# Performance work log

Hardware: AMD Instinct MI355X
Metric: run time of the kernel (lower is better)

## Reference

```python
import jax, jax.numpy as jnp
import numpy as np

# Model dims
L, B, S, D, H, V = 8, 4, 1024, 1024, 16, 256
FF = 4 * D
LN_EPS = 1e-5


def _ln(x, g, b):
    mu = jnp.mean(x, axis=-1, keepdims=True)
    var = jnp.mean(jnp.square(x - mu), axis=-1, keepdims=True)
    return (x - mu) * jax.lax.rsqrt(var + LN_EPS) * g + b


def setup_inputs() -> dict:
    key = jax.random.key(0)
    ks = jax.random.split(key, 12)
    p = lambda k, shape: (jax.random.normal(k, shape, jnp.float32) * 0.02)
    return {
        "input_tokens": jax.random.randint(ks[0], (B, S), 0, V),
        "tok_emb": p(ks[1], (V, D)),
        "pos_emb": p(ks[2], (S, D)),
        "Wq": p(ks[3], (L, D, D)),
        "Wk": p(ks[4], (L, D, D)),
        "Wv": p(ks[5], (L, D, D)),
        "Wo": p(ks[6], (L, D, D)),
        "bo": jnp.zeros((L, D), jnp.float32),
        "ln1_g": jnp.ones((L, D), jnp.float32),
        "ln1_b": jnp.zeros((L, D), jnp.float32),
        "ln2_g": jnp.ones((L, D), jnp.float32),
        "ln2_b": jnp.zeros((L, D), jnp.float32),
        "W1": p(ks[7], (L, D, FF)),
        "b1": jnp.zeros((L, FF), jnp.float32),
        "W2": p(ks[8], (L, FF, D)),
        "b2": jnp.zeros((L, D), jnp.float32),
        "lnf_g": jnp.ones((D,), jnp.float32),
        "lnf_b": jnp.zeros((D,), jnp.float32),
        "Wout": p(ks[9], (D, V)),
        "bout": jnp.zeros((V,), jnp.float32),
        "nhead": 16,
    }


def reference(input_tokens, tok_emb, pos_emb, Wq, Wk, Wv, Wo, bo,
              ln1_g, ln1_b, ln2_g, ln2_b, W1, b1, W2, b2,
              lnf_g, lnf_b, Wout, bout, nhead):
    b, s = input_tokens.shape
    d = tok_emb.shape[-1]
    hd = d // nhead
    scale = jnp.asarray(hd, jnp.float32) ** -0.5  # head_size ** -0.5
    mask = jnp.tril(jnp.ones((s, s), bool))  # causal

    x = tok_emb[input_tokens] + pos_emb[:s][None]  # [b,s,d]

    def block(x, p):
        wq, wk, wv, wo, bo_, g1, be1, g2, be2, w1, bf1, w2, bf2 = p
        h = _ln(x, g1, be1)
        q = (h @ wq).reshape(b, s, nhead, hd)
        k = (h @ wk).reshape(b, s, nhead, hd)
        v = (h @ wv).reshape(b, s, nhead, hd)
        scores = jnp.einsum('bqhd,bkhd->bhqk', q, k) * scale
        scores = jnp.where(mask, scores, -jnp.inf)
        attn = jax.nn.softmax(scores, axis=-1)  # dropout is identity (p=0 / eval)
        o = jnp.einsum('bhqk,bkhd->bqhd', attn, v).reshape(b, s, d)
        x = x + o @ wo + bo_
        h2 = _ln(x, g2, be2)
        x = x + jax.nn.relu(h2 @ w1 + bf1) @ w2 + bf2
        return x, None

    x, _ = jax.lax.scan(block, x, (Wq, Wk, Wv, Wo, bo, ln1_g, ln1_b,
                                   ln2_g, ln2_b, W1, b1, W2, b2))
    logits = _ln(x, lnf_g, lnf_b) @ Wout + bout  # [b,s,V]
    return logits
```

## Files before the change

### kernel.cpp

```cpp
#include <hip/hip_runtime.h>

#define DEV __device__ __forceinline__

typedef __bf16 bf16x8 __attribute__((ext_vector_type(8)));
typedef float  f32x4  __attribute__((ext_vector_type(4)));

typedef const __attribute__((address_space(1))) unsigned int* gas_ptr;
typedef       __attribute__((address_space(3))) unsigned int* las_ptr;

DEV unsigned short f2bf(float f) {
  union { __bf16 h; unsigned short u; } c; c.h = (__bf16)f; return c.u;
}

DEV float bf2f(unsigned short u) {
  union { unsigned int i; float f; } c; c.i = (unsigned int)u << 16; return c.f;
}

DEV void gll16(const void* g, void* l) {
  __builtin_amdgcn_global_load_lds((gas_ptr)g, (las_ptr)l, 16, 0, 0);
}

DEV f32x4 mfma16(bf16x8 a, bf16x8 b, f32x4 c) {
  return __builtin_amdgcn_mfma_f32_16x16x32_bf16(a, b, c, 0, 0, 0);
}

__global__ __launch_bounds__(256)
void tcvt_k(const float* __restrict__ src, unsigned short* __restrict__ dst,
            int K, int N)
{
  __shared__ float t[32][33];
  const int tx = threadIdx.x, ty = threadIdx.y;
  const size_t mo = (size_t)blockIdx.z * K * N;
  const int n0 = blockIdx.x * 32, k0 = blockIdx.y * 32;
  const float* s = src + mo;
  unsigned short* d = dst + mo;
#pragma unroll
  for (int i = 0; i < 4; i++)
    t[ty + i*8][tx] = s[(size_t)(k0 + ty + i*8) * N + n0 + tx];
  __syncthreads();
#pragma unroll
  for (int i = 0; i < 4; i++)
    d[(size_t)(n0 + ty + i*8) * K + k0 + tx] = f2bf(t[tx][ty + i*8]);
}

DEV void ln_tail(float4 s, const float* __restrict__ g,
                 const float* __restrict__ bta,
                 unsigned short* __restrict__ hrow, int t, float* red)
{
  float sm  = s.x + s.y + s.z + s.w;
  float sq = s.x*s.x + s.y*s.y + s.z*s.z + s.w*s.w;
#pragma unroll
  for (int mk = 32; mk >= 1; mk >>= 1) {
    sm += __shfl_xor(sm, mk);
    sq += __shfl_xor(sq, mk);
  }
  const int wv = t >> 6;
  if ((t & 63) == 0) { red[wv] = sm; red[4 + wv] = sq; }
  __syncthreads();
  sm = red[0] + red[1] + red[2] + red[3];
  sq = red[4] + red[5] + red[6] + red[7];
  const float mu = sm * (1.f/1024.f);
  const float rs = rsqrtf(sq * (1.f/1024.f) - mu*mu + 1e-5f);
  const float4 gv = ((const float4*)g)[t];
  const float4 bv = ((const float4*)bta)[t];
  ushort4 o;
  o.x = f2bf((s.x - mu) * rs * gv.x + bv.x);
  o.y = f2bf((s.y - mu) * rs * gv.y + bv.y);
  o.z = f2bf((s.z - mu) * rs * gv.z + bv.z);
  o.w = f2bf((s.w - mu) * rs * gv.w + bv.w);
  ((ushort4*)hrow)[t] = o;
}

__global__ __launch_bounds__(256)
void embed_ln_k(const int* __restrict__ toks, const float* __restrict__ te,
                const float* __restrict__ pe, const float* __restrict__ g,
                const float* __restrict__ bta,
                float* __restrict__ x, unsigned short* __restrict__ h)
{
  __shared__ float red[8];
  const int row = blockIdx.x, t = threadIdx.x;
  const int tok = toks[row], s = row & 1023;
  float4 a = ((const float4*)(te + (size_t)tok * 1024))[t];
  float4 p = ((const float4*)(pe + (size_t)s   * 1024))[t];
  float4 v; v.x = a.x+p.x; v.y = a.y+p.y; v.z = a.z+p.z; v.w = a.w+p.w;
  ((float4*)(x + (size_t)row * 1024))[t] = v;
  ln_tail(v, g, bta, h + (size_t)row * 1024, t, red);
}

__global__ __launch_bounds__(256)
void redln_k(const unsigned short* __restrict__ part,
             const float* __restrict__ bias,
             const float* __restrict__ g, const float* __restrict__ bta,
             float* __restrict__ x, unsigned short* __restrict__ h)
{
  __shared__ float red[8];
  const int row = blockIdx.x, t = threadIdx.x;
  const size_t pbase = (size_t)row * 1024 + t * 4;
  float a0 = 0.f, a1 = 0.f, a2 = 0.f, a3 = 0.f;
#pragma unroll
  for (int kz = 0; kz < 4; kz++) {
    ushort4 u = *(const ushort4*)&part[(size_t)kz * 4194304 + pbase];
    a0 += bf2f(u.x); a1 += bf2f(u.y); a2 += bf2f(u.z); a3 += bf2f(u.w);
  }
  float4 xv = ((const float4*)(x + (size_t)row * 1024))[t];
  float4 bv = ((const float4*)bias)[t];
  float4 s;
  s.x = xv.x + a0 + bv.x; s.y = xv.y + a1 + bv.y;
  s.z = xv.z + a2 + bv.z; s.w = xv.w + a3 + bv.w;
  ((float4*)(x + (size_t)row * 1024))[t] = s;
  ln_tail(s, g, bta, h + (size_t)row * 1024, t, red);
}

template<int EPI>
__global__ __launch_bounds__(256)
void gemm_k(const unsigned short* __restrict__ A,
            const unsigned short* __restrict__ B0,
            const unsigned short* __restrict__ B1,
            const unsigned short* __restrict__ B2,
            const float* __restrict__ bias,
            float* __restrict__ xio,
            unsigned short* __restrict__ o0,
            unsigned short* __restrict__ o1,
            unsigned short* __restrict__ o2,
            int K, int N, int Kc, float* __restrict__ part)
{
  __shared__ __align__(16) unsigned short As[2][128 * 32];
  __shared__ __align__(16) unsigned short Bs[2][128 * 32];
  const int tid = threadIdx.x;
  const int wave = tid >> 6, lane = tid & 63;
  const int wm = wave >> 1, wn = wave & 1;
  const int m0 = blockIdx.x * 128, n0 = blockIdx.y * 128;
  const int r16 = lane & 15, r4 = lane >> 4;

  const unsigned short* Bt = B0;
  if (EPI == 0) Bt = (blockIdx.z == 0) ? B0 : (blockIdx.z == 1) ? B1 : B2;
  const int koff = (EPI >= 4) ? blockIdx.z * Kc : 0;
  const int klen = (EPI >= 4) ? Kc : K;

  const unsigned short* ga = A  + (size_t)(m0 + (tid >> 2)) * K + koff + (tid & 3) * 8;
  const unsigned short* gb = Bt + (size_t)(n0 + (tid >> 2)) * K + koff + (tid & 3) * 8;
  const size_t rstep = (size_t)64 * K;
  const int lo = wave * 512;

  auto STAGE = [&](int slot, int tt) {
    const unsigned short* gaa = ga + tt * 32;
    const unsigned short* gbb = gb + tt * 32;
    gll16(gaa,         &As[slot][lo]);
    gll16(gaa + rstep, &As[slot][lo + 2048]);
    gll16(gbb,         &Bs[slot][lo]);
    gll16(gbb + rstep, &Bs[slot][lo + 2048]);
  };

  f32x4 acc[4][4] = {};
  const int NT = klen >> 5;

  STAGE(0, 0);
  if (NT > 1) STAGE(1, 1);

  for (int t = 0; t < NT; t++) {
    if (t + 1 < NT) asm volatile("s_waitcnt vmcnt(4)" ::: "memory");
    else            asm volatile("s_waitcnt vmcnt(0)" ::: "memory");
    __builtin_amdgcn_sched_barrier(0);
    __builtin_amdgcn_s_barrier();
    __builtin_amdgcn_sched_barrier(0);

    const int slot = t & 1;
    bf16x8 av[4], bv[4];
#pragma unroll
    for (int mf = 0; mf < 4; mf++)
      av[mf] = *(const bf16x8*)&As[slot][(wm*64 + mf*16 + r16) * 32 + r4 * 8];
#pragma unroll
    for (int nf = 0; nf < 4; nf++)
      bv[nf] = *(const bf16x8*)&Bs[slot][(wn*64 + nf*16 + r16) * 32 + r4 * 8];
    asm volatile("s_waitcnt lgkmcnt(0)" ::: "memory");
    __builtin_amdgcn_sched_barrier(0);
    __builtin_amdgcn_s_barrier();
    __builtin_amdgcn_sched_barrier(0);

    if (t + 2 < NT) STAGE(slot, t + 2);

#pragma unroll
    for (int mf = 0; mf < 4; mf++)
#pragma unroll
      for (int nf = 0; nf < 4; nf++)
        acc[mf][nf] = mfma16(av[mf], bv[nf], acc[mf][nf]);
    __builtin_amdgcn_sched_barrier(0);
  }

  const int row0 = m0 + wm * 64, col0 = n0 + wn * 64;
  float* po = nullptr;
  if (EPI == 4)
    po = part + (size_t)blockIdx.z * ((size_t)gridDim.x * 128 * N);
  unsigned short* po16 = nullptr;
  if (EPI == 5)
    po16 = o0 + (size_t)blockIdx.z * 4194304;
#pragma unroll
  for (int mf = 0; mf < 4; mf++) {
#pragma unroll
    for (int nf = 0; nf < 4; nf++) {
#pragma unroll
      for (int jj = 0; jj < 4; jj++) {
        const int r = row0 + mf*16 + r4*4 + jj;
        const int c = col0 + nf*16 + r16;
        const float v = acc[mf][nf][jj];
        if (EPI == 0) {
          const int z = blockIdx.z;
          const int b_ = r >> 10, s_ = r & 1023;
          const int hh = c >> 6, e = c & 63;
          if (z == 0)
            o0[((size_t)(b_*16 + hh) * 1024 + s_) * 64 + e] = f2bf(v * 0.125f);
          else if (z == 1)
            o1[((size_t)(b_*16 + hh) * 1024 + s_) * 64 + e] = f2bf(v);
          else
            o2[((size_t)(b_*16 + hh) * 64 + e) * 1024 + s_] = f2bf(v);
        } else if (EPI == 1) {
          const size_t idx = (size_t)r * N + c;
          xio[idx] += v + bias[c];
        } else if (EPI == 2) {
          const float t2 = v + bias[c];
          o0[(size_t)r * N + c] = f2bf(t2 > 0.f ? t2 : 0.f);
        } else if (EPI == 3) {
          xio[(size_t)r * N + c] = v + bias[c];
        } else if (EPI == 4) {
          po[(size_t)r * N + c] = v;
        } else {
          po16[(size_t)r * N + c] = f2bf(v);
        }
      }
    }
  }
}

__global__ __launch_bounds__(256)
void red_k(const float* __restrict__ part, const float* __restrict__ bias,
           float* __restrict__ outw, int n4, int nm4, int KZ)
{
  const float4* p4 = (const float4*)part;
  const float4* b4 = (const float4*)bias;
  for (size_t i = (size_t)blockIdx.x * 256 + threadIdx.x; i < (size_t)n4;
       i += (size_t)gridDim.x * 256) {
    float4 s = p4[i];
    for (int kz = 1; kz < KZ; kz++) {
      float4 t = p4[i + (size_t)kz * n4];
      s.x += t.x; s.y += t.y; s.z += t.z; s.w += t.w;
    }
    float4 bv = b4[i & nm4];
    s.x += bv.x; s.y += bv.y; s.z += bv.z; s.w += bv.w;
    ((float4*)outw)[i] = s;
  }
}

__global__ __launch_bounds__(256)
void attn_k(const unsigned short* __restrict__ qb,
            const unsigned short* __restrict__ kb,
            const unsigned short* __restrict__ vtb,
            unsigned short* __restrict__ att)
{
  __shared__ __align__(16) unsigned short Ks[2][64 * 64];
  __shared__ __align__(16) unsigned short Vs[2][64 * 64];
  __shared__ __align__(16) unsigned short Ps[64 * 72];
  const int flat = blockIdx.x;
  const int job  = (flat & 7) * 128 + (flat >> 3);
  const int qt   = 15 - (job & 15);
  const int h    = (job >> 4) & 15;
  const int b    = job >> 8;
  const int tid = threadIdx.x, wave = tid >> 6, lane = tid & 63;
  const int r16 = lane & 15, r4 = lane >> 4;
  const int q0 = qt * 64;
  const size_t bh = (size_t)(b * 16 + h);
  const unsigned short* qbh = qb  + bh * 1024 * 64;
  const unsigned short* kbh = kb  + bh * 1024 * 64;
  const unsigned short* vbh = vtb + bh * 64 * 1024;

  const int swz = ((lane & 7) ^ (lane >> 3)) * 8;
  const int srow = lane >> 3;

  auto STAGE = [&](int slot, int tt) {
    const int kv0 = tt * 64;
#pragma unroll
    for (int cc = 0; cc < 2; cc++) {
      const int chunk = wave * 2 + cc;
      gll16(kbh + (size_t)(kv0 + chunk*8 + srow) * 64 + swz,   &Ks[slot][chunk * 512]);
      gll16(vbh + (size_t)(chunk*8 + srow) * 1024 + kv0 + swz, &Vs[slot][chunk * 512]);
    }
  };

  bf16x8 qf[2];
#pragma unroll
  for (int kc = 0; kc < 2; kc++)
    qf[kc] = *(const bf16x8*)&qbh[(size_t)(q0 + wave*16 + r16) * 64 + kc*32 + r4*8];

  f32x4 oacc[4] = {};
  float l_i[4] = {0.f, 0.f, 0.f, 0.f};

  const int nt = qt + 1;

  STAGE(0, 0);
  if (nt > 1) STAGE(1, 1);

  for (int t = 0; t < nt; t++) {
    if (t + 1 < nt) asm volatile("s_waitcnt vmcnt(4)" ::: "memory");
    else            asm volatile("s_waitcnt vmcnt(0)" ::: "memory");
    __builtin_amdgcn_sched_barrier(0);
    __builtin_amdgcn_s_barrier();
    __builtin_amdgcn_sched_barrier(0);

    const int slot = t & 1;
    bf16x8 kf[2][4], vf[2][4];
#pragma unroll
    for (int kc = 0; kc < 2; kc++)
#pragma unroll
      for (int nf = 0; nf < 4; nf++) {
        kf[kc][nf] = *(const bf16x8*)&Ks[slot][(nf*16 + r16) * 64 +
                                              (((kc*4 + r4) ^ (r16 & 7)) * 8)];
        vf[kc][nf] = *(const bf16x8*)&Vs[slot][(nf*16 + r16) * 64 +
                                              (((kc*4 + r4) ^ (r16 & 7)) * 8)];
      }
    asm volatile("s_waitcnt lgkmcnt(0)" ::: "memory");
    __builtin_amdgcn_sched_barrier(0);
    __builtin_amdgcn_s_barrier();
    __builtin_amdgcn_sched_barrier(0);

    if (t + 2 < nt) STAGE(slot, t + 2);

    f32x4 sacc[4] = {};
#pragma unroll
    for (int kc = 0; kc < 2; kc++)
#pragma unroll
      for (int nf = 0; nf < 4; nf++)
        sacc[nf] = mfma16(qf[kc], kf[kc][nf], sacc[nf]);

    const bool diag = (t == nt - 1);
#pragma unroll
    for (int jj = 0; jj < 4; jj++) {
      float vv[4];
#pragma unroll
      for (int nf = 0; nf < 4; nf++) vv[nf] = sacc[nf][jj];
      if (diag) {
        const int qrow_l = wave*16 + r4*4 + jj;
#pragma unroll
        for (int nf = 0; nf < 4; nf++)
          if (nf*16 + r16 > qrow_l) vv[nf] = -1e30f;
      }
      float p0 = __expf(vv[0]), p1 = __expf(vv[1]);
      float p2 = __expf(vv[2]), p3 = __expf(vv[3]);
      l_i[jj] += (p0 + p1) + (p2 + p3);
      const int prow = (wave*16 + r4*4 + jj) * 72;
      Ps[prow + r16     ] = f2bf(p0);
      Ps[prow + 16 + r16] = f2bf(p1);
      Ps[prow + 32 + r16] = f2bf(p2);
      Ps[prow + 48 + r16] = f2bf(p3);
    }

#pragma unroll
    for (int kc = 0; kc < 2; kc++) {
      bf16x8 pf = *(const bf16x8*)&Ps[(wave*16 + r16) * 72 + kc*32 + r4*8];
#pragma unroll
      for (int nh = 0; nh < 4; nh++)
        oacc[nh] = mfma16(pf, vf[kc][nh], oacc[nh]);
    }
    __builtin_amdgcn_sched_barrier(0);
  }

#pragma unroll
  for (int jj = 0; jj < 4; jj++)
#pragma unroll
    for (int mk = 8; mk >= 1; mk >>= 1) l_i[jj] += __shfl_xor(l_i[jj], mk);

#pragma unroll
  for (int nh = 0; nh < 4; nh++) {
#pragma unroll
    for (int jj = 0; jj < 4; jj++) {
      const int row = q0 + wave*16 + r4*4 + jj;
      const int col = nh*16 + r16;
      const float o = oacc[nh][jj] / l_i[jj];
      att[(size_t)(b * 1024 + row) * 1024 + h*64 + col] = f2bf(o);
    }
  }
}

extern "C" void kernel_launch(void* const* d_in, const int* in_sizes, int n_in,
                              void* d_out, int out_size, void* d_ws, size_t ws_size,
                              hipStream_t stream)
{
  const int*   toks    = (const int*)  d_in[0];
  const float* tok_emb = (const float*)d_in[1];
  const float* pos_emb = (const float*)d_in[2];
  const float* Wq      = (const float*)d_in[3];
  const float* Wk      = (const float*)d_in[4];
  const float* Wv      = (const float*)d_in[5];
  const float* Wo      = (const float*)d_in[6];
  const float* bo      = (const float*)d_in[7];
  const float* ln1_g   = (const float*)d_in[8];
  const float* ln1_b   = (const float*)d_in[9];
  const float* ln2_g   = (const float*)d_in[10];
  const float* ln2_b   = (const float*)d_in[11];
  const float* W1      = (const float*)d_in[12];
  const float* b1      = (const float*)d_in[13];
  const float* W2      = (const float*)d_in[14];
  const float* b2      = (const float*)d_in[15];
  const float* lnf_g   = (const float*)d_in[16];
  const float* lnf_b   = (const float*)d_in[17];
  const float* Wout    = (const float*)d_in[18];
  const float* bout    = (const float*)d_in[19];
  float* out = (float*)d_out;

  char* w = (char*)d_ws;
  size_t off = 0;
  auto alloc = [&](size_t bytes) -> void* {
    void* p = w + off; off += (bytes + 255) & ~(size_t)255; return p;
  };
  unsigned short* wqT   = (unsigned short*)alloc(8ull*1024*1024*2);
  unsigned short* wkT   = (unsigned short*)alloc(8ull*1024*1024*2);
  unsigned short* wvT   = (unsigned short*)alloc(8ull*1024*1024*2);
  unsigned short* woT   = (unsigned short*)alloc(8ull*1024*1024*2);
  unsigned short* w1T   = (unsigned short*)alloc(8ull*1024*4096*2);
  unsigned short* w2T   = (unsigned short*)alloc(8ull*4096*1024*2);
  unsigned short* woutT = (unsigned short*)alloc(256ull*1024*2);
  float*          x     = (float*)         alloc(4096ull*1024*4);
  unsigned short* hbuf  = (unsigned short*)alloc(4096ull*1024*2);
  unsigned short* qbuf  = (unsigned short*)alloc(64ull*1024*64*2);
  unsigned short* kbuf  = (unsigned short*)alloc(64ull*1024*64*2);
  unsigned short* vtb   = (unsigned short*)alloc(64ull*1024*64*2);
  unsigned short* att   = (unsigned short*)alloc(4096ull*1024*2);
  unsigned short* ff    = (unsigned short*)alloc(4096ull*4096*2);
  unsigned short* part16= (unsigned short*)alloc(4ull*4194304*2);
  float*          part  = (float*)         alloc(8ull*1048576*4);
  (void)ws_size; (void)in_sizes; (void)n_in; (void)out_size;

  dim3 tb(32, 8);
  tcvt_k<<<dim3(32, 32, 8),  tb, 0, stream>>>(Wq,   wqT,   1024, 1024);
  tcvt_k<<<dim3(32, 32, 8),  tb, 0, stream>>>(Wk,   wkT,   1024, 1024);
  tcvt_k<<<dim3(32, 32, 8),  tb, 0, stream>>>(Wv,   wvT,   1024, 1024);
  tcvt_k<<<dim3(32, 32, 8),  tb, 0, stream>>>(Wo,   woT,   1024, 1024);
  tcvt_k<<<dim3(128, 32, 8), tb, 0, stream>>>(W1,   w1T,   1024, 4096);
  tcvt_k<<<dim3(32, 128, 8), tb, 0, stream>>>(W2,   w2T,   4096, 1024);
  tcvt_k<<<dim3(8, 32, 1),   tb, 0, stream>>>(Wout, woutT, 1024, 256);

  embed_ln_k<<<4096, 256, 0, stream>>>(toks, tok_emb, pos_emb,
                                       ln1_g, ln1_b, x, hbuf);

  for (int l = 0; l < 8; l++) {
    gemm_k<0><<<dim3(32, 8, 3), 256, 0, stream>>>(hbuf,
        wqT + (size_t)l*1048576, wkT + (size_t)l*1048576, wvT + (size_t)l*1048576,
        nullptr, nullptr, qbuf, kbuf, vtb, 1024, 1024, 1024, nullptr);
    attn_k<<<1024, 256, 0, stream>>>(qbuf, kbuf, vtb, att);
    gemm_k<5><<<dim3(32, 8, 4), 256, 0, stream>>>(att,
        woT + (size_t)l*1048576, nullptr, nullptr,
        nullptr, nullptr, part16, nullptr, nullptr, 1024, 1024, 256, nullptr);
    redln_k<<<4096, 256, 0, stream>>>(part16, bo + l*1024,
        ln2_g + l*1024, ln2_b + l*1024, x, hbuf);
    gemm_k<2><<<dim3(32, 32), 256, 0, stream>>>(hbuf,
        w1T + (size_t)l*4194304, nullptr, nullptr,
        b1 + l*4096, nullptr, ff, nullptr, nullptr, 1024, 4096, 1024, nullptr);
    gemm_k<5><<<dim3(32, 8, 4), 256, 0, stream>>>(ff,
        w2T + (size_t)l*4194304, nullptr, nullptr,
        nullptr, nullptr, part16, nullptr, nullptr, 4096, 1024, 1024, nullptr);
    if (l < 7)
      redln_k<<<4096, 256, 0, stream>>>(part16, b2 + l*1024,
          ln1_g + (l+1)*1024, ln1_b + (l+1)*1024, x, hbuf);
    else
      redln_k<<<4096, 256, 0, stream>>>(part16, b2 + l*1024,
          lnf_g, lnf_b, x, hbuf);
  }

  gemm_k<4><<<dim3(32, 2, 8), 256, 0, stream>>>(hbuf, woutT, nullptr, nullptr,
      nullptr, nullptr, nullptr, nullptr, nullptr, 1024, 256, 128, part);
  red_k<<<1024, 256, 0, stream>>>(part, bout, out, 262144, 63, 8);
}
```

Before: 2.059 ms.

## Add 256x256-tile 8-wave GEMM kernel for FFN matmuls

Introduces a new gemm8_k kernel with 512 threads and 256x256 output tiles. It double-buffers LDS through global_load_lds with XOR swizzling, interleaves the staging of A and B halves between MFMA phases, and raises wave priority around the MFMA bursts. The two FFN GEMMs (W1 with ReLU, and the split-K W2) now use it in place of the 128-tile kernel, to raise operand reuse per LDS byte and overlap loads with compute. Unused epilogues 1 and 3 are removed from the old kernel. The larger tiles give fewer blocks (256 for W1 and for W2), which risks worse occupancy and wave-quantization on the CUs, and the kernel needs heavy register use for 32 accumulators per lane.

```diff
diff --git a/kernel.cpp b/kernel.cpp
--- a/kernel.cpp
+++ b/kernel.cpp
@@ -213,16 +213,164 @@
             o1[((size_t)(b_*16 + hh) * 1024 + s_) * 64 + e] = f2bf(v);
           else
             o2[((size_t)(b_*16 + hh) * 64 + e) * 1024 + s_] = f2bf(v);
-        } else if (EPI == 1) {
-          const size_t idx = (size_t)r * N + c;
-          xio[idx] += v + bias[c];
         } else if (EPI == 2) {
           const float t2 = v + bias[c];
           o0[(size_t)r * N + c] = f2bf(t2 > 0.f ? t2 : 0.f);
-        } else if (EPI == 3) {
-          xio[(size_t)r * N + c] = v + bias[c];
         } else if (EPI == 4) {
           po[(size_t)r * N + c] = v;
+        } else if (EPI == 5) {
+          po16[(size_t)r * N + c] = f2bf(v);
+        }
+      }
+    }
+  }
+}
+
+template<int EPI>
+__global__ __launch_bounds__(512, 2)
+void gemm8_k(const unsigned short* __restrict__ A,
+             const unsigned short* __restrict__ Bt,
+             const float* __restrict__ bias,
+             unsigned short* __restrict__ o0,
+             int K, int N, int Kc)
+{
+  __shared__ __align__(16) unsigned short LA[2][2][8192];
+  __shared__ __align__(16) unsigned short LB[2][2][8192];
+  const int tid = threadIdx.x;
+  const int wave = tid >> 6, lane = tid & 63;
+  const int wm = wave >> 2, wn = wave & 3;
+  const int r16 = lane & 15, r4 = lane >> 4;
+  const int m0 = blockIdx.x * 256, n0 = blockIdx.y * 256;
+  const int koff = blockIdx.z * Kc;
+  const int NT = Kc >> 6;
+
+  const unsigned short* As0 = A  + (size_t)m0 * K + koff;
+  const unsigned short* As1 = A  + (size_t)(m0 + 128) * K + koff;
+  const unsigned short* Bs0 = Bt + (size_t)n0 * K + koff;
+  const unsigned short* Bs1 = Bt + (size_t)(n0 + 128) * K + koff;
+
+  auto STAGEH = [&](unsigned short* lds, const unsigned short* gsrc) {
+    const int c0 = tid, r0 = c0 >> 3;
+    gll16(gsrc + (size_t)r0 * K + ((c0 & 7) ^ (r0 & 7)) * 8, lds + c0 * 8);
+    const int c1 = 512 + tid, r1 = c1 >> 3;
+    gll16(gsrc + (size_t)r1 * K + ((c1 & 7) ^ (r1 & 7)) * 8, lds + c1 * 8);
+  };
+
+  f32x4 acc[8][4] = {};
+  bf16x8 avx[4][2], bvx[2][2][2];
+
+  STAGEH(&LB[0][0][0], Bs0);
+  STAGEH(&LB[0][1][0], Bs1);
+  STAGEH(&LA[0][0][0], As0);
+  STAGEH(&LA[0][1][0], As1);
+  if (NT > 1) {
+    STAGEH(&LB[1][0][0], Bs0 + 64);
+    STAGEH(&LB[1][1][0], Bs1 + 64);
+  }
+
+  for (int t = 0; t < NT; ++t) {
+    const int slot = t & 1;
+    if (t + 1 < NT) asm volatile("s_waitcnt vmcnt(4)" ::: "memory");
+    else            asm volatile("s_waitcnt vmcnt(0)" ::: "memory");
+    __builtin_amdgcn_sched_barrier(0);
+    __builtin_amdgcn_s_barrier();
+    __builtin_amdgcn_sched_barrier(0);
+
+#pragma unroll
+    for (int mfq = 0; mfq < 4; mfq++)
+#pragma unroll
+      for (int kk = 0; kk < 2; kk++)
+        avx[mfq][kk] = *(const bf16x8*)&LA[slot][wm][
+            (mfq*16 + r16) * 64 + (((kk*4 + r4) ^ (r16 & 7)) * 8)];
+#pragma unroll
+    for (int nfq = 0; nfq < 2; nfq++)
+#pragma unroll
+      for (int kk = 0; kk < 2; kk++)
+        bvx[0][nfq][kk] = *(const bf16x8*)&LB[slot][wn >> 1][
+            ((wn & 1)*64 + nfq*16 + r16) * 64 + (((kk*4 + r4) ^ (r16 & 7)) * 8)];
+    if (t + 1 < NT) STAGEH(&LA[slot ^ 1][0][0], As0 + (t + 1) * 64);
+    asm volatile("s_waitcnt lgkmcnt(0)" ::: "memory");
+    __builtin_amdgcn_sched_barrier(0);
+    __builtin_amdgcn_s_setprio(1);
+#pragma unroll
+    for (int mfq = 0; mfq < 4; mfq++)
+#pragma unroll
+      for (int nfq = 0; nfq < 2; nfq++)
+#pragma unroll
+        for (int kk = 0; kk < 2; kk++)
+          acc[mfq][nfq] = mfma16(avx[mfq][kk], bvx[0][nfq][kk], acc[mfq][nfq]);
+    __builtin_amdgcn_s_setprio(0);
+
+#pragma unroll
+    for (int nfq = 0; nfq < 2; nfq++)
+#pragma unroll
+      for (int kk = 0; kk < 2; kk++)
+        bvx[1][nfq][kk] = *(const bf16x8*)&LB[slot][wn >> 1][
+            ((wn & 1)*64 + 32 + nfq*16 + r16) * 64 + (((kk*4 + r4) ^ (r16 & 7)) * 8)];
+    if (t + 1 < NT) STAGEH(&LA[slot ^ 1][1][0], As1 + (t + 1) * 64);
+    asm volatile("s_waitcnt lgkmcnt(0)" ::: "memory");
+    __builtin_amdgcn_sched_barrier(0);
+    __builtin_amdgcn_s_setprio(1);
+#pragma unroll
+    for (int mfq = 0; mfq < 4; mfq++)
+#pragma unroll
+      for (int nfq = 0; nfq < 2; nfq++)
+#pragma unroll
+        for (int kk = 0; kk < 2; kk++)
+          acc[mfq][2 + nfq] = mfma16(avx[mfq][kk], bvx[1][nfq][kk], acc[mfq][2 + nfq]);
+    __builtin_amdgcn_s_setprio(0);
+
+    __builtin_amdgcn_sched_barrier(0);
+    __builtin_amdgcn_s_barrier();
+    __builtin_amdgcn_sched_barrier(0);
+
+#pragma unroll
+    for (int mfq = 0; mfq < 4; mfq++)
+#pragma unroll
+      for (int kk = 0; kk < 2; kk++)
+        avx[mfq][kk] = *(const bf16x8*)&LA[slot][wm][
+            (64 + mfq*16 + r16) * 64 + (((kk*4 + r4) ^ (r16 & 7)) * 8)];
+    if (t + 2 < NT) STAGEH(&LB[slot][0][0], Bs0 + (t + 2) * 64);
+    asm volatile("s_waitcnt lgkmcnt(0)" ::: "memory");
+    __builtin_amdgcn_sched_barrier(0);
+    __builtin_amdgcn_s_setprio(1);
+#pragma unroll
+    for (int mfq = 0; mfq < 4; mfq++)
+#pragma unroll
+      for (int nfq = 0; nfq < 2; nfq++)
+#pragma unroll
+        for (int kk = 0; kk < 2; kk++)
+          acc[4 + mfq][nfq] = mfma16(avx[mfq][kk], bvx[0][nfq][kk], acc[4 + mfq][nfq]);
+    __builtin_amdgcn_s_setprio(0);
+
+    if (t + 2 < NT) STAGEH(&LB[slot][1][0], Bs1 + (t + 2) * 64);
+    __builtin_amdgcn_s_setprio(1);
+#pragma unroll
+    for (int mfq = 0; mfq < 4; mfq++)
+#pragma unroll
+      for (int nfq = 0; nfq < 2; nfq++)
+#pragma unroll
+        for (int kk = 0; kk < 2; kk++)
+          acc[4 + mfq][2 + nfq] = mfma16(avx[mfq][kk], bvx[1][nfq][kk], acc[4 + mfq][2 + nfq]);
+    __builtin_amdgcn_s_setprio(0);
+    __builtin_amdgcn_sched_barrier(0);
+  }
+
+  const int row0 = m0 + wm * 128, col0 = n0 + wn * 64;
+  unsigned short* po16 = o0;
+  if (EPI == 5) po16 = o0 + (size_t)blockIdx.z * 4194304;
+#pragma unroll
+  for (int mf = 0; mf < 8; mf++) {
+#pragma unroll
+    for (int nf = 0; nf < 4; nf++) {
+#pragma unroll
+      for (int jj = 0; jj < 4; jj++) {
+        const int r = row0 + mf*16 + r4*4 + jj;
+        const int c = col0 + nf*16 + r16;
+        const float v = acc[mf][nf][jj];
+        if (EPI == 2) {
+          const float t2 = v + bias[c];
+          po16[(size_t)r * N + c] = f2bf(t2 > 0.f ? t2 : 0.f);
         } else {
           po16[(size_t)r * N + c] = f2bf(v);
         }
@@ -450,12 +598,10 @@
         nullptr, nullptr, part16, nullptr, nullptr, 1024, 1024, 256, nullptr);
     redln_k<<<4096, 256, 0, stream>>>(part16, bo + l*1024,
         ln2_g + l*1024, ln2_b + l*1024, x, hbuf);
-    gemm_k<2><<<dim3(32, 32), 256, 0, stream>>>(hbuf,
-        w1T + (size_t)l*4194304, nullptr, nullptr,
-        b1 + l*4096, nullptr, ff, nullptr, nullptr, 1024, 4096, 1024, nullptr);
-    gemm_k<5><<<dim3(32, 8, 4), 256, 0, stream>>>(ff,
-        w2T + (size_t)l*4194304, nullptr, nullptr,
-        nullptr, nullptr, part16, nullptr, nullptr, 4096, 1024, 1024, nullptr);
+    gemm8_k<2><<<dim3(16, 16), 512, 0, stream>>>(hbuf,
+        w1T + (size_t)l*4194304, b1 + l*4096, ff, 1024, 4096, 1024);
+    gemm8_k<5><<<dim3(16, 4, 4), 512, 0, stream>>>(ff,
+        w2T + (size_t)l*4194304, nullptr, part16, 4096, 1024, 1024);
     if (l < 7)
       redln_k<<<4096, 256, 0, stream>>>(part16, b2 + l*1024,
           ln1_g + (l+1)*1024, ln1_b + (l+1)*1024, x, hbuf);
```

Result: faster. 1.707 ms (-17.1%).
